# Kernel tuning notes

Measured on AMD Instinct MI355X. Metric: run time of the kernel, lower is better.

Reference implementation:

```python
import jax, jax.numpy as jnp
import numpy as np

B, T, E, H = 16, 4096, 384, 64

def setup_inputs() -> dict:
    key = jax.random.key(0)
    k1, k2, k3, k4 = jax.random.split(key, 4)
    x = jax.random.normal(k1, (B, T, E), dtype=jnp.float32)
    # nn.Linear default init ~ U(-1/sqrt(fan_in), 1/sqrt(fan_in)); scale normals similarly
    s = 1.0 / np.sqrt(E)
    Wk = jax.random.uniform(k2, (E, H), dtype=jnp.float32, minval=-s, maxval=s)
    Wq = jax.random.uniform(k3, (E, H), dtype=jnp.float32, minval=-s, maxval=s)
    Wv = jax.random.uniform(k4, (E, H), dtype=jnp.float32, minval=-s, maxval=s)
    return {"x": x, "Wk": Wk, "Wq": Wq, "Wv": Wv}

def reference(x, Wk, Wq, Wv):
    b, t, c = x.shape
    k = x @ Wk          # [b,t,h]
    q = x @ Wq          # [b,t,h]
    v = x @ Wv          # [b,t,h]
    # scale by C**-0.5 where C is the embedding dim (as in source)
    scale = c ** (-0.5)
    weights = jnp.einsum('bqh,bkh->bqk', q, k) * scale  # [b,t,t]
    causal = jnp.tril(jnp.ones((t, t), dtype=bool))
    weights = jnp.where(causal, weights, -jnp.inf)
    weights = jax.nn.softmax(weights, axis=-1)
    # dropout is identity in eval mode
    out = jnp.einsum('bqk,bkh->bqh', weights, v)          # [b,t,h]
    return out
```

## Files before the change

### kernel.cpp

```cpp
#include <hip/hip_runtime.h>
#include <hip/hip_bf16.h>
#include <math.h>


typedef __attribute__((ext_vector_type(4))) float f32x4;
typedef __attribute__((ext_vector_type(8))) __bf16 bf16x8;

#define DEVI static __device__ __forceinline__

DEVI unsigned short f2bf(float f) {
  union { float f; unsigned int u; } x; x.f = f;
  unsigned int r = x.u + 0x7fffu + ((x.u >> 16) & 1u);
  return (unsigned short)(r >> 16);
}

DEVI float bf2f(unsigned int u) {
  union { unsigned int u; float f; } x; x.u = u << 16;
  return x.f;
}

DEVI unsigned int cvtpk_bf16(float lo, float hi) {
  unsigned int r;
  asm("v_cvt_pk_bf16_f32 %0, %1, %2" : "=v"(r) : "v"(lo), "v"(hi));
  return r;
}

DEVI f32x4 mfma16(bf16x8 a, bf16x8 b, f32x4 c) {
  return __builtin_amdgcn_mfma_f32_16x16x32_bf16(a, b, c, 0, 0, 0);
}

DEVI bf16x8 lds_frag(const unsigned short* buf, int row, int gran) {
  return *(const bf16x8*)(buf + row * 64 + ((gran ^ (row & 7)) << 3));
}

DEVI void gl_lds16(const unsigned short* g, unsigned short* l) {
  __builtin_amdgcn_global_load_lds(
      (const __attribute__((address_space(1))) unsigned int*)g,
      (__attribute__((address_space(3))) unsigned int*)l, 16, 0, 0);
}

__global__ __launch_bounds__(256) void k_pack(const float* __restrict__ Wk,
                                              const float* __restrict__ Wq,
                                              const float* __restrict__ Wv,
                                              unsigned short* __restrict__ WT) {
  int idx = blockIdx.x * 256 + threadIdx.x;
  if (idx >= 192 * 384) return;
  int n = idx / 384, k = idx - n * 384;
  const float* W = (n < 64) ? Wk : ((n < 128) ? Wq : Wv);
  float val = W[k * 64 + (n & 63)];
  if (n >= 64 && n < 128) val *= 0.073622223f;
  WT[idx] = f2bf(val);
}

__global__ __launch_bounds__(256, 4) void k_proj(const float* __restrict__ x,
                                                 const unsigned short* __restrict__ WT,
                                                 unsigned short* __restrict__ Y,
                                                 unsigned short* __restrict__ VT) {
  __shared__ __align__(16) unsigned short As[64 * 64];
  __shared__ __align__(16) unsigned short Bs[192 * 64];
  const int tid = threadIdx.x;
  const int lane = tid & 63, wid = tid >> 6;
  const int q = lane & 15, g = lane >> 4;
  const int wm = wid >> 1, wn = wid & 1;
  const int m0 = blockIdx.x * 64;

  f32x4 acc[2][6];
#pragma unroll
  for (int mt = 0; mt < 2; ++mt)
#pragma unroll
    for (int nt = 0; nt < 6; ++nt) acc[mt][nt] = f32x4{0.f, 0.f, 0.f, 0.f};

  const int ar = tid >> 2, ap = tid & 3;

  for (int ks = 0; ks < 6; ++ks) {
    const float4* xp = (const float4*)(x + (size_t)(m0 + ar) * 384 + ks * 64 + ap * 16);
#pragma unroll
    for (int cc = 0; cc < 2; ++cc) {
      float4 f0 = xp[cc * 2], f1 = xp[cc * 2 + 1];
      union { unsigned short h[8]; uint4 v; } u;
      u.h[0] = f2bf(f0.x); u.h[1] = f2bf(f0.y); u.h[2] = f2bf(f0.z); u.h[3] = f2bf(f0.w);
      u.h[4] = f2bf(f1.x); u.h[5] = f2bf(f1.y); u.h[6] = f2bf(f1.z); u.h[7] = f2bf(f1.w);
      int gran = ap * 2 + cc;
      *(uint4*)(As + ar * 64 + ((gran ^ (ar & 7)) << 3)) = u.v;
    }
#pragma unroll
    for (int i = 0; i < 6; ++i) {
      int c = tid + 256 * i;
      int row = c >> 3, gr = c & 7;
      uint4 w = *(const uint4*)(WT + (size_t)row * 384 + ks * 64 + gr * 8);
      *(uint4*)(Bs + row * 64 + ((gr ^ (row & 7)) << 3)) = w;
    }
    __syncthreads();
#pragma unroll
    for (int kk = 0; kk < 2; ++kk) {
      bf16x8 af[2], bfv[6];
#pragma unroll
      for (int mt = 0; mt < 2; ++mt) af[mt] = lds_frag(As, wm * 32 + mt * 16 + q, kk * 4 + g);
#pragma unroll
      for (int nt = 0; nt < 6; ++nt) bfv[nt] = lds_frag(Bs, wn * 96 + nt * 16 + q, kk * 4 + g);
#pragma unroll
      for (int mt = 0; mt < 2; ++mt)
#pragma unroll
        for (int nt = 0; nt < 6; ++nt) acc[mt][nt] = mfma16(af[mt], bfv[nt], acc[mt][nt]);
    }
    __syncthreads();
  }
#pragma unroll
  for (int mt = 0; mt < 2; ++mt) {
    const int mrow = m0 + wm * 32 + mt * 16 + g * 4;
#pragma unroll
    for (int nt = 0; nt < 6; ++nt) {
      const int ncol = wn * 96 + nt * 16 + q;
      if (wn == 1 && nt >= 2) {
        const int d = (nt - 2) * 16 + q;
        const int bb = mrow >> 12, t = mrow & 4095;
        uint2 pv;
        pv.x = cvtpk_bf16(acc[mt][nt][0], acc[mt][nt][1]);
        pv.y = cvtpk_bf16(acc[mt][nt][2], acc[mt][nt][3]);
        *(uint2*)(VT + (size_t)(bb * 64 + d) * 4096 + t) = pv;
      } else {
        size_t base = (size_t)mrow * 128 + ncol;
#pragma unroll
        for (int j = 0; j < 4; ++j) Y[base + (size_t)j * 128] = f2bf(acc[mt][nt][j]);
      }
    }
  }
}

__global__ __launch_bounds__(512, 4) void k_attn(const unsigned short* __restrict__ Y,
                                                 const unsigned short* __restrict__ VT,
                                                 unsigned short* __restrict__ PO,
                                                 float* __restrict__ PL) {
  __shared__ __align__(16) unsigned short Ks[4][64 * 64];
  __shared__ __align__(16) unsigned short Vs[4][64 * 64];

  const int id = blockIdx.x;
  const int xcd = id & 7;
  const int b = xcd * 2 + ((id >> 3) & 1);
  const int idx = id >> 4;
  const int i = 31 - (idx >> 1);
  const int h = idx & 1;
  const int nIt = i + 1, nH0 = (nIt + 1) >> 1;
  const int itBeg = h ? nH0 : 0;
  const int itEnd = h ? nIt : nH0;
  const int q0 = i * 128;
  const int tEnd = 2 * itEnd;

  const int tid = threadIdx.x;
  const int lane = tid & 63, wid = tid >> 6;
  const int p = wid >> 2;
  const int w4 = wid & 3;
  const int q = lane & 15, g = lane >> 4;

  const unsigned short* Yb = Y + (size_t)b * 4096 * 128;
  const unsigned short* Vb = VT + (size_t)b * 64 * 4096;

#define STAGE(S, KV0)                                                           \
  {                                                                             \
    int r = tid >> 3, grs = (tid & 7) ^ (r & 7);                                \
    int kp = (r & 32) | ((r & 12) << 1) | ((r & 16) >> 2) | (r & 3);            \
    gl_lds16(Yb + (size_t)((KV0) + kp) * 128 + grs * 8, Ks[S] + tid * 8);       \
    gl_lds16(Vb + (size_t)r * 4096 + (KV0) + grs * 8, Vs[S] + tid * 8);         \
  }

  {
    const int tb = 2 * itBeg;
    STAGE(tb & 3, tb * 64)
    STAGE((tb + 1) & 3, (tb + 1) * 64)
  }
  __syncthreads();

  bf16x8 qf[2][2];
#pragma unroll
  for (int qh = 0; qh < 2; ++qh) {
    const unsigned short* qp = Yb + (size_t)(q0 + w4 * 32 + qh * 16 + q) * 128 + 64;
    qf[qh][0] = *(const bf16x8*)(qp + g * 8);
    qf[qh][1] = *(const bf16x8*)(qp + 32 + g * 8);
  }

  f32x4 accO[2][4];
#pragma unroll
  for (int qh = 0; qh < 2; ++qh)
#pragma unroll
    for (int dt = 0; dt < 4; ++dt) accO[qh][dt] = f32x4{0.f, 0.f, 0.f, 0.f};
  float lsum[2] = {0.f, 0.f};

  const int mytiles = 2 * i + 1 + (w4 >> 1);

  for (int it = itBeg; it < itEnd; ++it) {
    const int kt = 2 * it + p;
    const int t2 = 2 * it + 2, t3 = 2 * it + 3;
    if (t2 < tEnd) STAGE(t2 & 3, t2 * 64)
    if (t3 < tEnd) STAGE(t3 & 3, t3 * 64)

    if (kt < mytiles) {
      const int kv0 = kt * 64;
      const unsigned short* Kc = Ks[kt & 3];
      const unsigned short* Vc = Vs[kt & 3];

      bf16x8 ka0[4], ka1[4];
#pragma unroll
      for (int t = 0; t < 4; ++t) {
        ka0[t] = lds_frag(Kc, t * 16 + q, g);
        ka1[t] = lds_frag(Kc, t * 16 + q, 4 + g);
      }
      f32x4 accS[2][4];
      __builtin_amdgcn_s_setprio(1);
#pragma unroll
      for (int qh = 0; qh < 2; ++qh)
#pragma unroll
        for (int t = 0; t < 4; ++t) {
          f32x4 z = f32x4{0.f, 0.f, 0.f, 0.f};
          z = mfma16(ka0[t], qf[qh][0], z);
          z = mfma16(ka1[t], qf[qh][1], z);
          accS[qh][t] = z;
        }
      __builtin_amdgcn_s_setprio(0);

      const bool dmw = (kv0 + 63 >= q0 + w4 * 32);
      bf16x8 bp[2][2];
#pragma unroll
      for (int qh = 0; qh < 2; ++qh) {
        if (dmw) {
          const int qrow = q0 + w4 * 32 + qh * 16 + q;
#pragma unroll
          for (int t = 0; t < 4; ++t)
#pragma unroll
            for (int j = 0; j < 4; ++j) {
              const int kvl = ((t >> 1) << 5) + (g << 3) + ((t & 1) << 2) + j;
              if (kv0 + kvl > qrow) accS[qh][t][j] = -INFINITY;
            }
        }
        float pp[4][4];
        float ps0 = 0.f, ps1 = 0.f;
#pragma unroll
        for (int t = 0; t < 4; ++t) {
          pp[t][0] = __builtin_amdgcn_exp2f(accS[qh][t][0]);
          pp[t][1] = __builtin_amdgcn_exp2f(accS[qh][t][1]);
          pp[t][2] = __builtin_amdgcn_exp2f(accS[qh][t][2]);
          pp[t][3] = __builtin_amdgcn_exp2f(accS[qh][t][3]);
          ps0 += pp[t][0] + pp[t][1];
          ps1 += pp[t][2] + pp[t][3];
        }
        lsum[qh] += ps0 + ps1;
        uint4 u0, u1;
        u0.x = cvtpk_bf16(pp[0][0], pp[0][1]);
        u0.y = cvtpk_bf16(pp[0][2], pp[0][3]);
        u0.z = cvtpk_bf16(pp[1][0], pp[1][1]);
        u0.w = cvtpk_bf16(pp[1][2], pp[1][3]);
        u1.x = cvtpk_bf16(pp[2][0], pp[2][1]);
        u1.y = cvtpk_bf16(pp[2][2], pp[2][3]);
        u1.z = cvtpk_bf16(pp[3][0], pp[3][1]);
        u1.w = cvtpk_bf16(pp[3][2], pp[3][3]);
        bp[qh][0] = __builtin_bit_cast(bf16x8, u0);
        bp[qh][1] = __builtin_bit_cast(bf16x8, u1);
      }

      __builtin_amdgcn_s_setprio(1);
#pragma unroll
      for (int dt = 0; dt < 4; ++dt) {
        bf16x8 av0 = lds_frag(Vc, dt * 16 + q, g);
        bf16x8 av1 = lds_frag(Vc, dt * 16 + q, 4 + g);
#pragma unroll
        for (int qh = 0; qh < 2; ++qh) {
          accO[qh][dt] = mfma16(av0, bp[qh][0], accO[qh][dt]);
          accO[qh][dt] = mfma16(av1, bp[qh][1], accO[qh][dt]);
        }
      }
      __builtin_amdgcn_s_setprio(0);
    }

    __syncthreads();
  }
#undef STAGE

#pragma unroll
  for (int qh = 0; qh < 2; ++qh) {
    lsum[qh] += __shfl_xor(lsum[qh], 16);
    lsum[qh] += __shfl_xor(lsum[qh], 32);
  }

  float* scrO = (float*)Ks;
  float* scrL = (float*)Vs;
  const int si = (w4 * 64 + lane) * 2;
  if (p == 1) {
#pragma unroll
    for (int qh = 0; qh < 2; ++qh) {
      float* so = scrO + (si + qh) * 16;
#pragma unroll
      for (int dt = 0; dt < 4; ++dt) *(float4*)(so + dt * 4) = *(float4*)&accO[qh][dt];
      scrL[si + qh] = lsum[qh];
    }
  }
  __syncthreads();
  if (p == 0) {
    const int jobj = (b << 5) + i;
    unsigned short* PO_ = PO + ((size_t)(jobj * 2 + h)) * 8192;
    float* PL_ = PL + (jobj * 2 + h) * 128;
#pragma unroll
    for (int qh = 0; qh < 2; ++qh) {
      const float* so = scrO + (si + qh) * 16;
      const float lt = lsum[qh] + scrL[si + qh];
      const int row = w4 * 32 + qh * 16 + q;
      if (g == 0) PL_[row] = lt;
#pragma unroll
      for (int dt = 0; dt < 4; ++dt) {
        float4 ob = *(const float4*)(so + dt * 4);
        uint2 pv;
        pv.x = cvtpk_bf16(accO[qh][dt][0] + ob.x, accO[qh][dt][1] + ob.y);
        pv.y = cvtpk_bf16(accO[qh][dt][2] + ob.z, accO[qh][dt][3] + ob.w);
        *(uint2*)(PO_ + row * 64 + dt * 16 + g * 4) = pv;
      }
    }
  }
}

__global__ __launch_bounds__(256) void k_red(const unsigned short* __restrict__ PO,
                                             const float* __restrict__ PL,
                                             float* __restrict__ out) {
  const int idx = blockIdx.x * 256 + threadIdx.x;
  const int dq = idx & 15;
  const int row = (idx >> 4) & 127;
  const int j = idx >> 11;
  const int b = j >> 5, i = j & 31;

  const unsigned short* a0 = PO + ((size_t)(j * 2)) * 8192 + row * 64 + dq * 4;
  const uint2 u0 = *(const uint2*)a0;
  const uint2 u1 = *(const uint2*)(a0 + 8192);
  const float rl = 1.0f / (PL[(j * 2) * 128 + row] + PL[(j * 2 + 1) * 128 + row]);

  float4 o;
  o.x = (bf2f(u0.x & 0xffffu) + bf2f(u1.x & 0xffffu)) * rl;
  o.y = (bf2f(u0.x >> 16) + bf2f(u1.x >> 16)) * rl;
  o.z = (bf2f(u0.y & 0xffffu) + bf2f(u1.y & 0xffffu)) * rl;
  o.w = (bf2f(u0.y >> 16) + bf2f(u1.y >> 16)) * rl;
  *(float4*)(out + ((size_t)(b * 4096 + i * 128 + row)) * 64 + dq * 4) = o;
}

extern "C" void kernel_launch(void* const* d_in, const int* in_sizes, int n_in,
                              void* d_out, int out_size, void* d_ws, size_t ws_size,
                              hipStream_t stream) {
  const float* x  = (const float*)d_in[0];
  const float* Wk = (const float*)d_in[1];
  const float* Wq = (const float*)d_in[2];
  const float* Wv = (const float*)d_in[3];
  float* out = (float*)d_out;

  unsigned short* WT = (unsigned short*)d_ws;
  unsigned short* Y  = WT + 73728;
  unsigned short* VT = Y + 8388608;
  unsigned short* PO = VT + 4194304;
  float*          PL = (float*)(PO + 8388608);

  hipLaunchKernelGGL(k_pack, dim3(288), dim3(256), 0, stream, Wk, Wq, Wv, WT);
  hipLaunchKernelGGL(k_proj, dim3(1024), dim3(256), 0, stream, x, WT, Y, VT);
  hipLaunchKernelGGL(k_attn, dim3(1024), dim3(512), 0, stream, Y, VT, PO, PL);
  hipLaunchKernelGGL(k_red, dim3(4096), dim3(256), 0, stream, PO, PL, out);
}
```

Baseline: 84.56 us.

## Fuse split-K reduction into attention kernel via last-block atomic flag

```diff
diff --git a/kernel.cpp b/kernel.cpp
--- a/kernel.cpp
+++ b/kernel.cpp
@@ -77,11 +77,13 @@
 #pragma unroll
     for (int cc = 0; cc < 2; ++cc) {
       float4 f0 = xp[cc * 2], f1 = xp[cc * 2 + 1];
-      union { unsigned short h[8]; uint4 v; } u;
-      u.h[0] = f2bf(f0.x); u.h[1] = f2bf(f0.y); u.h[2] = f2bf(f0.z); u.h[3] = f2bf(f0.w);
-      u.h[4] = f2bf(f1.x); u.h[5] = f2bf(f1.y); u.h[6] = f2bf(f1.z); u.h[7] = f2bf(f1.w);
+      uint4 v;
+      v.x = cvtpk_bf16(f0.x, f0.y);
+      v.y = cvtpk_bf16(f0.z, f0.w);
+      v.z = cvtpk_bf16(f1.x, f1.y);
+      v.w = cvtpk_bf16(f1.z, f1.w);
       int gran = ap * 2 + cc;
-      *(uint4*)(As + ar * 64 + ((gran ^ (ar & 7)) << 3)) = u.v;
+      *(uint4*)(As + ar * 64 + ((gran ^ (ar & 7)) << 3)) = v;
     }
 #pragma unroll
     for (int i = 0; i < 6; ++i) {
@@ -130,9 +132,12 @@
 __global__ __launch_bounds__(512, 4) void k_attn(const unsigned short* __restrict__ Y,
                                                  const unsigned short* __restrict__ VT,
                                                  unsigned short* __restrict__ PO,
-                                                 float* __restrict__ PL) {
+                                                 float* __restrict__ PL,
+                                                 int* __restrict__ flags,
+                                                 float* __restrict__ out) {
   __shared__ __align__(16) unsigned short Ks[4][64 * 64];
   __shared__ __align__(16) unsigned short Vs[4][64 * 64];
+  __shared__ int lastFlag;
 
   const int id = blockIdx.x;
   const int xcd = id & 7;
@@ -293,8 +298,8 @@
     }
   }
   __syncthreads();
+  const int jobj = (b << 5) + i;
   if (p == 0) {
-    const int jobj = (b << 5) + i;
     unsigned short* PO_ = PO + ((size_t)(jobj * 2 + h)) * 8192;
     float* PL_ = PL + (jobj * 2 + h) * 128;
 #pragma unroll
@@ -313,28 +318,31 @@
       }
     }
   }
-}
-
-__global__ __launch_bounds__(256) void k_red(const unsigned short* __restrict__ PO,
-                                             const float* __restrict__ PL,
-                                             float* __restrict__ out) {
-  const int idx = blockIdx.x * 256 + threadIdx.x;
-  const int dq = idx & 15;
-  const int row = (idx >> 4) & 127;
-  const int j = idx >> 11;
-  const int b = j >> 5, i = j & 31;
-
-  const unsigned short* a0 = PO + ((size_t)(j * 2)) * 8192 + row * 64 + dq * 4;
-  const uint2 u0 = *(const uint2*)a0;
-  const uint2 u1 = *(const uint2*)(a0 + 8192);
-  const float rl = 1.0f / (PL[(j * 2) * 128 + row] + PL[(j * 2 + 1) * 128 + row]);
-
-  float4 o;
-  o.x = (bf2f(u0.x & 0xffffu) + bf2f(u1.x & 0xffffu)) * rl;
-  o.y = (bf2f(u0.x >> 16) + bf2f(u1.x >> 16)) * rl;
-  o.z = (bf2f(u0.y & 0xffffu) + bf2f(u1.y & 0xffffu)) * rl;
-  o.w = (bf2f(u0.y >> 16) + bf2f(u1.y >> 16)) * rl;
-  *(float4*)(out + ((size_t)(b * 4096 + i * 128 + row)) * 64 + dq * 4) = o;
+
+  __syncthreads();
+  if (tid == 0) {
+    lastFlag = __hip_atomic_fetch_add(&flags[jobj], 1, __ATOMIC_ACQ_REL,
+                                      __HIP_MEMORY_SCOPE_AGENT);
+  }
+  __syncthreads();
+  if (lastFlag == 1) {
+    const size_t base = (size_t)(jobj * 2) * 8192;
+#pragma unroll
+    for (int r2 = 0; r2 < 4; ++r2) {
+      const int item = tid + r2 * 512;
+      const int dq = item & 15, row = item >> 4;
+      const unsigned short* a0 = PO + base + row * 64 + dq * 4;
+      const uint2 u0 = *(const uint2*)a0;
+      const uint2 u1 = *(const uint2*)(a0 + 8192);
+      const float rl = 1.0f / (PL[(jobj * 2) * 128 + row] + PL[(jobj * 2 + 1) * 128 + row]);
+      float4 o;
+      o.x = (bf2f(u0.x & 0xffffu) + bf2f(u1.x & 0xffffu)) * rl;
+      o.y = (bf2f(u0.x >> 16) + bf2f(u1.x >> 16)) * rl;
+      o.z = (bf2f(u0.y & 0xffffu) + bf2f(u1.y & 0xffffu)) * rl;
+      o.w = (bf2f(u0.y >> 16) + bf2f(u1.y >> 16)) * rl;
+      *(float4*)(out + ((size_t)(b * 4096 + q0 + row)) * 64 + dq * 4) = o;
+    }
+  }
 }
 
 extern "C" void kernel_launch(void* const* d_in, const int* in_sizes, int n_in,
@@ -351,9 +359,10 @@
   unsigned short* VT = Y + 8388608;
   unsigned short* PO = VT + 4194304;
   float*          PL = (float*)(PO + 8388608);
-
+  int*            FL = (int*)(PL + 131072);
+
+  hipMemsetAsync(FL, 0, 512 * sizeof(int), stream);
   hipLaunchKernelGGL(k_pack, dim3(288), dim3(256), 0, stream, Wk, Wq, Wv, WT);
   hipLaunchKernelGGL(k_proj, dim3(1024), dim3(256), 0, stream, x, WT, Y, VT);
-  hipLaunchKernelGGL(k_attn, dim3(1024), dim3(512), 0, stream, Y, VT, PO, PL);
-  hipLaunchKernelGGL(k_red, dim3(4096), dim3(256), 0, stream, PO, PL, out);
-}
+  hipLaunchKernelGGL(k_attn, dim3(1024), dim3(512), 0, stream, Y, VT, PO, PL, FL, out);
+}
```

Result: slower. 118.9 us (+40.6%).
